# Performance work log

Hardware: AMD Instinct MI355X
Metric: run time of the kernel (lower is better)

The kernel has to match this reference:

```python
import jax, jax.numpy as jnp
import numpy as np

D = 128          # fine voxel grid resolution
N0 = 250000
D_IN, D_BASE, D_OUT = 16, 8, 8
EPS = 1e-5
# (cin, cout) for conv0..conv6, conv7, conv9, conv11
_CH = [(16, 8), (8, 16), (16, 16), (16, 32), (32, 32), (32, 64), (64, 64), (64, 32), (32, 16), (16, 8)]

def _offsets():
    r = np.arange(-1, 2)
    return np.stack(np.meshgrid(r, r, r, indexing='ij'), -1).reshape(-1, 3)  # [27,3]

def _lookup_fn(coords, d):
    keys = (coords[:, 0].astype(np.int64) * d + coords[:, 1]) * d + coords[:, 2]
    order = np.argsort(keys)
    skeys = keys[order]
    def lookup(q):
        valid = ((q >= 0) & (q < d)).all(-1)
        k = (q[:, 0].astype(np.int64) * d + q[:, 1]) * d + q[:, 2]
        pos = np.clip(np.searchsorted(skeys, k), 0, len(skeys) - 1)
        return np.where(valid & (skeys[pos] == k), order[pos], -1).astype(np.int32)
    return lookup

def _nbr_same(coords, d):
    # stride-1 sparse conv: outputs at input coords, neighbors at coord+k
    lk = _lookup_fn(coords, d)
    return np.stack([lk(coords + o) for o in _offsets()], 1)  # [N,27]

def _nbr_down(c_out, c_in, d_in):
    # stride-2 conv: output p gathers inputs at 2p+k
    lk = _lookup_fn(c_in, d_in)
    return np.stack([lk(c_out * 2 + o) for o in _offsets()], 1)

def _nbr_up(c_out, c_in, d_in):
    # transposed stride-2 conv: output q gathers input p=(q-k)/2 where divisible
    lk = _lookup_fn(c_in, d_in)
    cols = []
    for o in _offsets():
        q = c_out - o
        div = (q % 2 == 0).all(-1)
        cols.append(np.where(div, lk(q // 2), -1).astype(np.int32))
    return np.stack(cols, 1)

def setup_inputs():
    rng = np.random.default_rng(0)
    flat = rng.choice(D ** 3, size=N0, replace=False)
    c0 = np.stack([flat // (D * D), (flat // D) % D, flat % D], 1).astype(np.int32)
    c1 = np.unique(c0 // 2, axis=0)
    c2 = np.unique(c1 // 2, axis=0)
    c3 = np.unique(c2 // 2, axis=0)
    inp = {
        'feats': jax.random.normal(jax.random.key(0), (N0, D_IN), jnp.float32),
        'nbr0': jnp.asarray(_nbr_same(c0, D)),
        'nbr_d01': jnp.asarray(_nbr_down(c1, c0, D)),
        'nbr1': jnp.asarray(_nbr_same(c1, D // 2)),
        'nbr_d12': jnp.asarray(_nbr_down(c2, c1, D // 2)),
        'nbr2': jnp.asarray(_nbr_same(c2, D // 4)),
        'nbr_d23': jnp.asarray(_nbr_down(c3, c2, D // 4)),
        'nbr3': jnp.asarray(_nbr_same(c3, D // 8)),
        'nbr_u32': jnp.asarray(_nbr_up(c2, c3, D // 8)),
        'nbr_u21': jnp.asarray(_nbr_up(c1, c2, D // 4)),
        'nbr_u10': jnp.asarray(_nbr_up(c0, c1, D // 2)),
    }
    key = jax.random.key(1)
    for i, (ci, co) in enumerate(_CH):
        key, kw = jax.random.split(key)
        inp['w%d' % i] = jax.random.normal(kw, (27, ci, co), jnp.float32) / np.sqrt(27.0 * ci)
        inp['g%d' % i] = jnp.ones((co,), jnp.float32)
        inp['b%d' % i] = jnp.zeros((co,), jnp.float32)
    inp['lin_w'] = jax.random.normal(jax.random.key(2), (D_OUT, D_BASE), jnp.float32) / np.sqrt(D_BASE)
    return inp

def _sconv_bn_relu(f, nbr, w, g, b):
    # f: [Nin,Cin], nbr: [Nout,27] (-1 = no neighbor), w: [27,Cin,Cout]
    gth = jnp.where((nbr >= 0)[..., None], f[jnp.maximum(nbr, 0)], 0.0)  # [Nout,27,Cin]
    y = jnp.einsum('nkc,kco->no', gth, w)
    mu = y.mean(0)                       # training-mode BatchNorm over active voxels
    var = y.var(0)
    return jax.nn.relu((y - mu) * jax.lax.rsqrt(var + EPS) * g + b)

def reference(feats, nbr0, nbr_d01, nbr1, nbr_d12, nbr2, nbr_d23, nbr3, nbr_u32, nbr_u21, nbr_u10,
              w0, g0, b0, w1, g1, b1, w2, g2, b2, w3, g3, b3, w4, g4, b4,
              w5, g5, b5, w6, g6, b6, w7, g7, b7, w8, g8, b8, w9, g9, b9, lin_w):
    c0f = _sconv_bn_relu(feats, nbr0, w0, g0, b0)
    c2f = _sconv_bn_relu(_sconv_bn_relu(c0f, nbr_d01, w1, g1, b1), nbr1, w2, g2, b2)
    c4f = _sconv_bn_relu(_sconv_bn_relu(c2f, nbr_d12, w3, g3, b3), nbr2, w4, g4, b4)
    x = _sconv_bn_relu(_sconv_bn_relu(c4f, nbr_d23, w5, g5, b5), nbr3, w6, g6, b6)
    x = c4f + _sconv_bn_relu(x, nbr_u32, w7, g7, b7)
    x = c2f + _sconv_bn_relu(x, nbr_u21, w8, g8, b8)
    x = c0f + _sconv_bn_relu(x, nbr_u10, w9, g9, b9)
    return x @ lin_w.T, x
```

## Files before the change

### kernel.cpp

```cpp
#include <hip/hip_runtime.h>

#define EPSV 1e-5f

typedef __attribute__((ext_vector_type(8))) short short8;
typedef __attribute__((ext_vector_type(4))) float float4v;

static inline int cdiv(int a, int b) { return (a + b - 1) / b; }
static inline int imin(int a, int b) { return a < b ? a : b; }

__device__ inline unsigned short f2bf(float x) {
  unsigned u = __float_as_uint(x);
  return (unsigned short)((u + 0x7FFFu + ((u >> 16) & 1u)) >> 16);
}
__device__ inline float bf2f(unsigned short u) {
  return __uint_as_float(((unsigned)u) << 16);
}

#define NBUCKET 64

struct PrepArgs {
  const float* w[10];
  unsigned short* wt[10];
  int ci[10];
  int co[10];
  int wcum[11];
  const float* feats;
  unsigned short* featsb;
  int nfeat4;
  float* stats;
};

__global__ __launch_bounds__(256) void prep_kernel(PrepArgs p, long total) {
  const int nstat4 = 10 * NBUCKET * 128 / 4;
  for (long tid0 = (long)blockIdx.x * 256 + threadIdx.x; tid0 < total;
       tid0 += (long)gridDim.x * 256) {
    long tid = tid0;
    if (tid < nstat4) {
      ((float4*)p.stats)[tid] = make_float4(0.f, 0.f, 0.f, 0.f);
      continue;
    }
    tid -= nstat4;
    if (tid < p.nfeat4) {
      float4 v = ((const float4*)p.feats)[tid];
      ushort4 r;
      r.x = f2bf(v.x); r.y = f2bf(v.y); r.z = f2bf(v.z); r.w = f2bf(v.w);
      ((ushort4*)p.featsb)[tid] = r;
      continue;
    }
    tid -= p.nfeat4;
    if (tid >= p.wcum[10]) continue;
    int i = 0;
    while (tid >= p.wcum[i + 1]) ++i;
    int e = (int)(tid - p.wcum[i]);
    int ci = p.ci[i], co = p.co[i];
    int k = e / (ci * co);
    int r = e - k * (ci * co);
    int o = r / ci;
    int c = r - o * ci;
    p.wt[i][((long)k * co + o) * ci + c] = f2bf(p.w[i][((long)k * ci + c) * co + o]);
  }
}

template<int CI, int CO>
__global__ __launch_bounds__(256) void conv_mfma(
    const unsigned short* __restrict__ f, const int* __restrict__ nbr,
    const unsigned short* __restrict__ wt, unsigned short* __restrict__ y,
    float* __restrict__ stats, int nout, int ntiles) {
  constexpr int NCHUNK = (CI == 8) ? 7 : (CI == 16) ? 14 : (CI == 32) ? 27 : 54;

  const int tid = threadIdx.x;
  const int lane = tid & 63;
  const int wid = tid >> 6;
  const int m = lane & 15;
  const int quad = lane >> 4;
  const int cbase = blockIdx.y * 16;
  const int co = cbase + m;
  const bool cok = co < CO;

  auto tapof = [&](int c) -> int {
    if constexpr (CI == 8) return c * 4 + quad;
    else if constexpr (CI == 16) return c * 2 + (quad >> 1);
    else if constexpr (CI == 32) return c;
    else return c >> 1;
  };
  auto cioof = [&](int c) -> int {
    if constexpr (CI == 8) return 0;
    else if constexpr (CI == 16) return (quad & 1) * 8;
    else if constexpr (CI == 32) return quad * 8;
    else return ((c & 1) << 5) + quad * 8;
  };

  float sum = 0.f, sq = 0.f;

  if constexpr (CI <= 16) {
    short8 Bv[NCHUNK];
#pragma unroll
    for (int c = 0; c < NCHUNK; ++c) {
      int tap = tapof(c);
      short8 bq;
#pragma unroll
      for (int q = 0; q < 8; ++q) bq[q] = 0;
      if (cok && tap < 27) bq = *(const short8*)(wt + ((long)tap * CO + co) * CI + cioof(c));
      Bv[c] = bq;
    }
    for (int tile = blockIdx.x; tile < ntiles; tile += gridDim.x) {
      const int rowb = tile * 64 + wid * 16;
      const int row = rowb + m;
      const bool rok = row < nout;
      int idxs[NCHUNK];
#pragma unroll
      for (int c = 0; c < NCHUNK; ++c) {
        int tap = tapof(c);
        idxs[c] = (rok && tap < 27) ? nbr[(long)row * 27 + tap] : -1;
      }
      short8 A[NCHUNK];
#pragma unroll
      for (int c = 0; c < NCHUNK; ++c) {
        short8 a;
#pragma unroll
        for (int q = 0; q < 8; ++q) a[q] = 0;
        if (idxs[c] >= 0) a = *(const short8*)(f + (long)idxs[c] * CI + cioof(c));
        A[c] = a;
      }
      float4v acc = {0.f, 0.f, 0.f, 0.f};
#pragma unroll
      for (int c = 0; c < NCHUNK; ++c)
        acc = __builtin_amdgcn_mfma_f32_16x16x32_bf16(A[c], Bv[c], acc, 0, 0, 0);
#pragma unroll
      for (int r = 0; r < 4; ++r) {
        float v = acc[r];
        int orow = rowb + quad * 4 + r;
        if (cok && orow < nout) y[(long)orow * CO + co] = f2bf(v);
        sum += v;
        sq = fmaf(v, v, sq);
      }
    }
  } else {
    constexpr int G = 9;
    constexpr int NG = NCHUNK / G;
    for (int tile = blockIdx.x; tile < ntiles; tile += gridDim.x) {
      const int rowb = tile * 64 + wid * 16;
      const int row = rowb + m;
      const bool rok = row < nout;
      int idxs[27];
#pragma unroll
      for (int t = 0; t < 27; ++t)
        idxs[t] = rok ? nbr[(long)row * 27 + t] : -1;

      short8 A[2][G], B[2][G];
      auto load_group = [&](int g, int bi) {
#pragma unroll
        for (int j = 0; j < G; ++j) {
          const int c = g * G + j;
          const int tap = tapof(c);
          short8 a, bq;
#pragma unroll
          for (int q = 0; q < 8; ++q) { a[q] = 0; bq[q] = 0; }
          int idx = idxs[tap];
          if (idx >= 0) a = *(const short8*)(f + (long)idx * CI + cioof(c));
          if (cok) bq = *(const short8*)(wt + ((long)tap * CO + co) * CI + cioof(c));
          A[bi][j] = a; B[bi][j] = bq;
        }
      };
      float4v acc = {0.f, 0.f, 0.f, 0.f};
      load_group(0, 0);
#pragma unroll
      for (int g = 0; g < NG; ++g) {
        const int cur = g & 1;
        if (g + 1 < NG) load_group(g + 1, cur ^ 1);
#pragma unroll
        for (int j = 0; j < G; ++j)
          acc = __builtin_amdgcn_mfma_f32_16x16x32_bf16(A[cur][j], B[cur][j], acc, 0, 0, 0);
      }
#pragma unroll
      for (int r = 0; r < 4; ++r) {
        float v = acc[r];
        int orow = rowb + quad * 4 + r;
        if (cok && orow < nout) y[(long)orow * CO + co] = f2bf(v);
        sum += v;
        sq = fmaf(v, v, sq);
      }
    }
  }

  sum += __shfl_xor(sum, 16); sq += __shfl_xor(sq, 16);
  sum += __shfl_xor(sum, 32); sq += __shfl_xor(sq, 32);
  if (quad == 0 && cok) {
    float* st = stats + ((((unsigned)blockIdx.x * 4 + wid) & (NBUCKET - 1)) << 7);
    atomicAdd(&st[co], sum);
    atomicAdd(&st[64 + co], sq);
  }
}

template<int CO>
__global__ __launch_bounds__(256) void bn_relu_bf16(
    const unsigned short* __restrict__ y, const float* __restrict__ stats,
    const float* __restrict__ g, const float* __restrict__ b,
    const unsigned short* __restrict__ skip, unsigned short* __restrict__ out,
    int nout, float inv_n) {
  __shared__ float sA[CO], sC[CO];
  if ((int)threadIdx.x < CO) {
    int o = threadIdx.x;
    float su = 0.f, sq = 0.f;
#pragma unroll 8
    for (int bk = 0; bk < NBUCKET; ++bk) {
      su += stats[bk * 128 + o];
      sq += stats[bk * 128 + 64 + o];
    }
    float mu = su * inv_n;
    float var = sq * inv_n - mu * mu;
    float a = g[o] * rsqrtf(var + EPSV);
    sA[o] = a;
    sC[o] = fmaf(-mu, a, b[o]);
  }
  __syncthreads();
  long total4 = (long)nout * CO / 4;
  for (long i4 = (long)blockIdx.x * 256 + threadIdx.x; i4 < total4;
       i4 += (long)gridDim.x * 256) {
    int o = (int)((i4 * 4) % CO);
    ushort4 v = ((const ushort4*)y)[i4];
    float vv[4] = {bf2f(v.x), bf2f(v.y), bf2f(v.z), bf2f(v.w)};
    unsigned short rr[4];
#pragma unroll
    for (int j = 0; j < 4; ++j) {
      float x = fmaxf(fmaf(vv[j], sA[o + j], sC[o + j]), 0.f);
      if (skip) x += bf2f(skip[i4 * 4 + j]);
      rr[j] = f2bf(x);
    }
    ushort4 r;
    r.x = rr[0]; r.y = rr[1]; r.z = rr[2]; r.w = rr[3];
    ((ushort4*)out)[i4] = r;
  }
}

__global__ __launch_bounds__(256) void tail_kernel(
    const unsigned short* __restrict__ c0f, const float* __restrict__ st9,
    const float* __restrict__ g9, const float* __restrict__ b9, float inv_n,
    const float* __restrict__ lin_w, const unsigned short* __restrict__ y9,
    float* __restrict__ out0, float* __restrict__ x0, int n0) {
  __shared__ float swl[64];
  __shared__ float sbn[16];
  if (threadIdx.x < 64) swl[threadIdx.x] = lin_w[threadIdx.x];
  if (threadIdx.x < 8) {
    int o = threadIdx.x;
    float su = 0.f, sq = 0.f;
#pragma unroll 8
    for (int bk = 0; bk < NBUCKET; ++bk) {
      su += st9[bk * 128 + o];
      sq += st9[bk * 128 + 64 + o];
    }
    float mu = su * inv_n;
    float var = sq * inv_n - mu * mu;
    float a = g9[o] * rsqrtf(var + EPSV);
    sbn[o] = a;
    sbn[8 + o] = fmaf(-mu, a, b9[o]);
  }
  __syncthreads();
  for (int n = blockIdx.x * 256 + threadIdx.x; n < n0; n += gridDim.x * 256) {
    const ushort4* pr = (const ushort4*)(y9 + (long)n * 8);
    ushort4 r0 = pr[0], r1 = pr[1];
    unsigned short rw[8] = {r0.x, r0.y, r0.z, r0.w, r1.x, r1.y, r1.z, r1.w};
    const ushort4* pc = (const ushort4*)(c0f + (long)n * 8);
    ushort4 c0 = pc[0], c1 = pc[1];
    unsigned short cs[8] = {c0.x, c0.y, c0.z, c0.w, c1.x, c1.y, c1.z, c1.w};
    float xv[8];
#pragma unroll
    for (int c = 0; c < 8; ++c)
      xv[c] = bf2f(cs[c]) + fmaxf(fmaf(bf2f(rw[c]), sbn[c], sbn[8 + c]), 0.f);
    *(float4*)(x0 + (long)n * 8) = make_float4(xv[0], xv[1], xv[2], xv[3]);
    *(float4*)(x0 + (long)n * 8 + 4) = make_float4(xv[4], xv[5], xv[6], xv[7]);
    float ov[8];
#pragma unroll
    for (int j = 0; j < 8; ++j) {
      float s = 0.f;
#pragma unroll
      for (int c = 0; c < 8; ++c) s = fmaf(xv[c], swl[j * 8 + c], s);
      ov[j] = s;
    }
    *(float4*)(out0 + (long)n * 8) = make_float4(ov[0], ov[1], ov[2], ov[3]);
    *(float4*)(out0 + (long)n * 8 + 4) = make_float4(ov[4], ov[5], ov[6], ov[7]);
  }
}

extern "C" void kernel_launch(void* const* d_in, const int* in_sizes, int n_in,
                              void* d_out, int out_size, void* d_ws, size_t ws_size,
                              hipStream_t stream) {
  const float* feats   = (const float*)d_in[0];
  const int* nbr0      = (const int*)d_in[1];
  const int* nbr_d01   = (const int*)d_in[2];
  const int* nbr1      = (const int*)d_in[3];
  const int* nbr_d12   = (const int*)d_in[4];
  const int* nbr2      = (const int*)d_in[5];
  const int* nbr_d23   = (const int*)d_in[6];
  const int* nbr3      = (const int*)d_in[7];
  const int* nbr_u32   = (const int*)d_in[8];
  const int* nbr_u21   = (const int*)d_in[9];
  const int* nbr_u10   = (const int*)d_in[10];
  const float* w[10];
  const float* g[10];
  const float* b[10];
  for (int i = 0; i < 10; ++i) {
    w[i] = (const float*)d_in[11 + 3 * i];
    g[i] = (const float*)d_in[12 + 3 * i];
    b[i] = (const float*)d_in[13 + 3 * i];
  }
  const float* lin_w = (const float*)d_in[41];

  const int N0 = in_sizes[0] / 16;
  const int N1 = in_sizes[2] / 27;
  const int N2 = in_sizes[4] / 27;
  const int N3 = in_sizes[6] / 27;
  const float i0 = 1.f / N0, i1 = 1.f / N1, i2 = 1.f / N2, i3 = 1.f / N3;

  static const int CIv[10] = {16, 8, 16, 16, 32, 32, 64, 64, 32, 16};
  static const int COv[10] = {8, 16, 16, 32, 32, 64, 64, 32, 16, 8};

  float* stats = (float*)d_ws;
  unsigned short* u = (unsigned short*)(stats + 10 * NBUCKET * 128);

  unsigned short* yraw = u; u += (size_t)N1 * 32;

  unsigned short* wt[10];
  int wcum[11];
  wcum[0] = 0;
  for (int i = 0; i < 10; ++i) {
    wt[i] = u;
    int sz = 27 * CIv[i] * COv[i];
    u += sz;
    wcum[i + 1] = wcum[i] + sz;
  }
  unsigned short* featsb = u; u += (size_t)N0 * 16;
  unsigned short* c0f = u;    u += (size_t)N0 * 8;
  unsigned short* t1  = u;    u += (size_t)N1 * 16;
  unsigned short* c2f = u;    u += (size_t)N1 * 16;
  unsigned short* t2  = u;    u += (size_t)N2 * 32;
  unsigned short* c4f = u;    u += (size_t)N2 * 32;
  unsigned short* t3  = u;    u += (size_t)N3 * 64;
  unsigned short* t4  = u;    u += (size_t)N3 * 64;
  unsigned short* t5  = t2;
  unsigned short* t6  = t1;
  float* out0 = (float*)d_out;
  float* x0   = (float*)d_out + (size_t)N0 * 8;

  float* s[10];
  for (int i = 0; i < 10; ++i) s[i] = stats + i * NBUCKET * 128;

  PrepArgs pa;
  for (int i = 0; i < 10; ++i) {
    pa.w[i] = w[i]; pa.wt[i] = wt[i];
    pa.ci[i] = CIv[i]; pa.co[i] = COv[i];
    pa.wcum[i] = wcum[i];
  }
  pa.wcum[10] = wcum[10];
  pa.feats = feats; pa.featsb = featsb;
  pa.nfeat4 = N0 * 16 / 4;
  pa.stats = stats;
  long prep_total = (10 * NBUCKET * 128 / 4) + pa.nfeat4 + wcum[10];
  prep_kernel<<<imin((int)((prep_total + 255) / 256), 2048), 256, 0, stream>>>(pa, prep_total);

  auto bgrid = [](long nout, int co) {
    return imin((int)((nout * co / 4 + 255) / 256), 1024);
  };
  auto cgrid = [](int ntiles) { return imin(ntiles, 1024); };

  int tb0 = cdiv(N0, 64), tb1 = cdiv(N1, 64), tb2 = cdiv(N2, 64), tb3 = cdiv(N3, 64);

  conv_mfma<16, 8><<<dim3(cgrid(tb0), 1), 256, 0, stream>>>(featsb, nbr0, wt[0], yraw, s[0], N0, tb0);
  bn_relu_bf16<8><<<bgrid(N0, 8), 256, 0, stream>>>(yraw, s[0], g[0], b[0], nullptr, c0f, N0, i0);

  conv_mfma<8, 16><<<dim3(cgrid(tb1), 1), 256, 0, stream>>>(c0f, nbr_d01, wt[1], yraw, s[1], N1, tb1);
  bn_relu_bf16<16><<<bgrid(N1, 16), 256, 0, stream>>>(yraw, s[1], g[1], b[1], nullptr, t1, N1, i1);

  conv_mfma<16, 16><<<dim3(cgrid(tb1), 1), 256, 0, stream>>>(t1, nbr1, wt[2], yraw, s[2], N1, tb1);
  bn_relu_bf16<16><<<bgrid(N1, 16), 256, 0, stream>>>(yraw, s[2], g[2], b[2], nullptr, c2f, N1, i1);

  conv_mfma<16, 32><<<dim3(cgrid(tb2), 2), 256, 0, stream>>>(c2f, nbr_d12, wt[3], yraw, s[3], N2, tb2);
  bn_relu_bf16<32><<<bgrid(N2, 32), 256, 0, stream>>>(yraw, s[3], g[3], b[3], nullptr, t2, N2, i2);

  conv_mfma<32, 32><<<dim3(cgrid(tb2), 2), 256, 0, stream>>>(t2, nbr2, wt[4], yraw, s[4], N2, tb2);
  bn_relu_bf16<32><<<bgrid(N2, 32), 256, 0, stream>>>(yraw, s[4], g[4], b[4], nullptr, c4f, N2, i2);

  conv_mfma<32, 64><<<dim3(cgrid(tb3), 4), 256, 0, stream>>>(c4f, nbr_d23, wt[5], yraw, s[5], N3, tb3);
  bn_relu_bf16<64><<<bgrid(N3, 64), 256, 0, stream>>>(yraw, s[5], g[5], b[5], nullptr, t3, N3, i3);

  conv_mfma<64, 64><<<dim3(cgrid(tb3), 4), 256, 0, stream>>>(t3, nbr3, wt[6], yraw, s[6], N3, tb3);
  bn_relu_bf16<64><<<bgrid(N3, 64), 256, 0, stream>>>(yraw, s[6], g[6], b[6], nullptr, t4, N3, i3);

  conv_mfma<64, 32><<<dim3(cgrid(tb2), 2), 256, 0, stream>>>(t4, nbr_u32, wt[7], yraw, s[7], N2, tb2);
  bn_relu_bf16<32><<<bgrid(N2, 32), 256, 0, stream>>>(yraw, s[7], g[7], b[7], c4f, t5, N2, i2);

  conv_mfma<32, 16><<<dim3(cgrid(tb1), 1), 256, 0, stream>>>(t5, nbr_u21, wt[8], yraw, s[8], N1, tb1);
  bn_relu_bf16<16><<<bgrid(N1, 16), 256, 0, stream>>>(yraw, s[8], g[8], b[8], c2f, t6, N1, i1);

  conv_mfma<16, 8><<<dim3(cgrid(tb0), 1), 256, 0, stream>>>(t6, nbr_u10, wt[9], yraw, s[9], N0, tb0);

  tail_kernel<<<imin(cdiv(N0, 256), 1024), 256, 0, stream>>>(
      c0f, s[9], g[9], b[9], i0, lin_w, yraw, out0, x0, N0);
}
```

Measured before the change: 488.3 us.

## Stage conv weights and neighbor tiles in LDS, raise occupancy and grid size

The conv kernel now copies its slice of transposed weights into shared memory once per block, with an XOR swizzle for CI=64, and reads B fragments from LDS instead of keeping them in registers or reloading them from global memory on every tile. Each tile's 64x27 neighbor indices are loaded coalesced into shared memory with int4 loads. Launch bounds gain a per-instantiation min-waves hint and the conv grid cap rises from 1024 to 2048 blocks. In exchange it adds two __syncthreads per tile and LDS traffic, and the LDS footprint may limit occupancy.

```diff
diff --git a/kernel.cpp b/kernel.cpp
--- a/kernel.cpp
+++ b/kernel.cpp
@@ -61,12 +61,16 @@
   }
 }
 
-template<int CI, int CO>
-__global__ __launch_bounds__(256) void conv_mfma(
+template<int CI, int CO, int MINW>
+__global__ __launch_bounds__(256, MINW) void conv_mfma(
     const unsigned short* __restrict__ f, const int* __restrict__ nbr,
     const unsigned short* __restrict__ wt, unsigned short* __restrict__ y,
     float* __restrict__ stats, int nout, int ntiles) {
   constexpr int NCHUNK = (CI == 8) ? 7 : (CI == 16) ? 14 : (CI == 32) ? 27 : 54;
+  constexpr int CIP = (CI == 64) ? 64 : (CI == 32) ? 40 : 24;
+
+  __shared__ int nbrT[64 * 27];
+  __shared__ unsigned short Bs[27 * 16 * CIP];
 
   const int tid = threadIdx.x;
   const int lane = tid & 63;
@@ -89,29 +93,65 @@
     else if constexpr (CI == 32) return quad * 8;
     else return ((c & 1) << 5) + quad * 8;
   };
+  auto baddr = [&](int tap, int mm, int cio) -> int {
+    if constexpr (CI == 64) {
+      int byt = (tap * 16 + mm) * 128 + cio * 2;
+      byt ^= (mm & 7) << 4;
+      return byt >> 1;
+    } else {
+      return (tap * 16 + mm) * CIP + cio;
+    }
+  };
+
+  {
+    constexpr int NC8 = CI / 8;
+    for (int t = tid; t < 27 * 16 * NC8; t += 256) {
+      int tap = t / (16 * NC8);
+      int r = t - tap * (16 * NC8);
+      int mo = r / NC8;
+      int c8 = (r - mo * NC8) * 8;
+      short8 v;
+#pragma unroll
+      for (int q = 0; q < 8; ++q) v[q] = 0;
+      int c = cbase + mo;
+      if (c < CO) v = *(const short8*)(wt + ((long)tap * CO + c) * CI + c8);
+      *(short8*)&Bs[baddr(tap, mo, c8)] = v;
+    }
+  }
 
   float sum = 0.f, sq = 0.f;
 
-  if constexpr (CI <= 16) {
-    short8 Bv[NCHUNK];
-#pragma unroll
-    for (int c = 0; c < NCHUNK; ++c) {
-      int tap = tapof(c);
-      short8 bq;
-#pragma unroll
-      for (int q = 0; q < 8; ++q) bq[q] = 0;
-      if (cok && tap < 27) bq = *(const short8*)(wt + ((long)tap * CO + co) * CI + cioof(c));
-      Bv[c] = bq;
-    }
-    for (int tile = blockIdx.x; tile < ntiles; tile += gridDim.x) {
-      const int rowb = tile * 64 + wid * 16;
-      const int row = rowb + m;
-      const bool rok = row < nout;
+  for (int tile = blockIdx.x; tile < ntiles; tile += gridDim.x) {
+    const int rowb0 = tile * 64;
+    {
+      const int base = rowb0 * 27;
+      const int lim = nout * 27;
+      for (int j = tid; j < 432; j += 256) {
+        int e = j * 4;
+        int g = base + e;
+        int4 v;
+        if (g + 4 <= lim) {
+          v = *(const int4*)(nbr + g);
+        } else {
+          v.x = (g + 0 < lim) ? nbr[g + 0] : -1;
+          v.y = (g + 1 < lim) ? nbr[g + 1] : -1;
+          v.z = (g + 2 < lim) ? nbr[g + 2] : -1;
+          v.w = (g + 3 < lim) ? nbr[g + 3] : -1;
+        }
+        *(int4*)&nbrT[e] = v;
+      }
+    }
+    __syncthreads();
+
+    const int rowb = rowb0 + wid * 16;
+    const int lrow = (wid * 16 + m) * 27;
+
+    if constexpr (CI <= 16) {
       int idxs[NCHUNK];
 #pragma unroll
       for (int c = 0; c < NCHUNK; ++c) {
         int tap = tapof(c);
-        idxs[c] = (rok && tap < 27) ? nbr[(long)row * 27 + tap] : -1;
+        idxs[c] = (tap < 27) ? nbrT[lrow + tap] : -1;
       }
       short8 A[NCHUNK];
 #pragma unroll
@@ -124,8 +164,12 @@
       }
       float4v acc = {0.f, 0.f, 0.f, 0.f};
 #pragma unroll
-      for (int c = 0; c < NCHUNK; ++c)
-        acc = __builtin_amdgcn_mfma_f32_16x16x32_bf16(A[c], Bv[c], acc, 0, 0, 0);
+      for (int c = 0; c < NCHUNK; ++c) {
+        int tap = tapof(c);
+        int tapc = tap < 27 ? tap : 26;
+        short8 bf = *(const short8*)&Bs[baddr(tapc, m, cioof(c))];
+        acc = __builtin_amdgcn_mfma_f32_16x16x32_bf16(A[c], bf, acc, 0, 0, 0);
+      }
 #pragma unroll
       for (int r = 0; r < 4; ++r) {
         float v = acc[r];
@@ -134,32 +178,21 @@
         sum += v;
         sq = fmaf(v, v, sq);
       }
-    }
-  } else {
-    constexpr int G = 9;
-    constexpr int NG = NCHUNK / G;
-    for (int tile = blockIdx.x; tile < ntiles; tile += gridDim.x) {
-      const int rowb = tile * 64 + wid * 16;
-      const int row = rowb + m;
-      const bool rok = row < nout;
-      int idxs[27];
-#pragma unroll
-      for (int t = 0; t < 27; ++t)
-        idxs[t] = rok ? nbr[(long)row * 27 + t] : -1;
-
-      short8 A[2][G], B[2][G];
+    } else {
+      constexpr int G = 9;
+      constexpr int NG = NCHUNK / G;
+      short8 A[2][G];
       auto load_group = [&](int g, int bi) {
 #pragma unroll
         for (int j = 0; j < G; ++j) {
           const int c = g * G + j;
           const int tap = tapof(c);
-          short8 a, bq;
-#pragma unroll
-          for (int q = 0; q < 8; ++q) { a[q] = 0; bq[q] = 0; }
-          int idx = idxs[tap];
+          int idx = nbrT[lrow + tap];
+          short8 a;
+#pragma unroll
+          for (int q = 0; q < 8; ++q) a[q] = 0;
           if (idx >= 0) a = *(const short8*)(f + (long)idx * CI + cioof(c));
-          if (cok) bq = *(const short8*)(wt + ((long)tap * CO + co) * CI + cioof(c));
-          A[bi][j] = a; B[bi][j] = bq;
+          A[bi][j] = a;
         }
       };
       float4v acc = {0.f, 0.f, 0.f, 0.f};
@@ -169,8 +202,11 @@
         const int cur = g & 1;
         if (g + 1 < NG) load_group(g + 1, cur ^ 1);
 #pragma unroll
-        for (int j = 0; j < G; ++j)
-          acc = __builtin_amdgcn_mfma_f32_16x16x32_bf16(A[cur][j], B[cur][j], acc, 0, 0, 0);
+        for (int j = 0; j < G; ++j) {
+          const int c = g * G + j;
+          short8 bf = *(const short8*)&Bs[baddr(tapof(c), m, cioof(c))];
+          acc = __builtin_amdgcn_mfma_f32_16x16x32_bf16(A[cur][j], bf, acc, 0, 0, 0);
+        }
       }
 #pragma unroll
       for (int r = 0; r < 4; ++r) {
@@ -181,6 +217,7 @@
         sq = fmaf(v, v, sq);
       }
     }
+    __syncthreads();
   }
 
   sum += __shfl_xor(sum, 16); sq += __shfl_xor(sq, 16);
@@ -361,38 +398,38 @@
   auto bgrid = [](long nout, int co) {
     return imin((int)((nout * co / 4 + 255) / 256), 1024);
   };
-  auto cgrid = [](int ntiles) { return imin(ntiles, 1024); };
+  auto cgrid = [](int ntiles) { return imin(ntiles, 2048); };
 
   int tb0 = cdiv(N0, 64), tb1 = cdiv(N1, 64), tb2 = cdiv(N2, 64), tb3 = cdiv(N3, 64);
 
-  conv_mfma<16, 8><<<dim3(cgrid(tb0), 1), 256, 0, stream>>>(featsb, nbr0, wt[0], yraw, s[0], N0, tb0);
+  conv_mfma<16, 8, 4><<<dim3(cgrid(tb0), 1), 256, 0, stream>>>(featsb, nbr0, wt[0], yraw, s[0], N0, tb0);
   bn_relu_bf16<8><<<bgrid(N0, 8), 256, 0, stream>>>(yraw, s[0], g[0], b[0], nullptr, c0f, N0, i0);
 
-  conv_mfma<8, 16><<<dim3(cgrid(tb1), 1), 256, 0, stream>>>(c0f, nbr_d01, wt[1], yraw, s[1], N1, tb1);
+  conv_mfma<8, 16, 4><<<dim3(cgrid(tb1), 1), 256, 0, stream>>>(c0f, nbr_d01, wt[1], yraw, s[1], N1, tb1);
   bn_relu_bf16<16><<<bgrid(N1, 16), 256, 0, stream>>>(yraw, s[1], g[1], b[1], nullptr, t1, N1, i1);
 
-  conv_mfma<16, 16><<<dim3(cgrid(tb1), 1), 256, 0, stream>>>(t1, nbr1, wt[2], yraw, s[2], N1, tb1);
+  conv_mfma<16, 16, 4><<<dim3(cgrid(tb1), 1), 256, 0, stream>>>(t1, nbr1, wt[2], yraw, s[2], N1, tb1);
   bn_relu_bf16<16><<<bgrid(N1, 16), 256, 0, stream>>>(yraw, s[2], g[2], b[2], nullptr, c2f, N1, i1);
 
-  conv_mfma<16, 32><<<dim3(cgrid(tb2), 2), 256, 0, stream>>>(c2f, nbr_d12, wt[3], yraw, s[3], N2, tb2);
+  conv_mfma<16, 32, 4><<<dim3(cgrid(tb2), 2), 256, 0, stream>>>(c2f, nbr_d12, wt[3], yraw, s[3], N2, tb2);
   bn_relu_bf16<32><<<bgrid(N2, 32), 256, 0, stream>>>(yraw, s[3], g[3], b[3], nullptr, t2, N2, i2);
 
-  conv_mfma<32, 32><<<dim3(cgrid(tb2), 2), 256, 0, stream>>>(t2, nbr2, wt[4], yraw, s[4], N2, tb2);
+  conv_mfma<32, 32, 3><<<dim3(cgrid(tb2), 2), 256, 0, stream>>>(t2, nbr2, wt[4], yraw, s[4], N2, tb2);
   bn_relu_bf16<32><<<bgrid(N2, 32), 256, 0, stream>>>(yraw, s[4], g[4], b[4], nullptr, c4f, N2, i2);
 
-  conv_mfma<32, 64><<<dim3(cgrid(tb3), 4), 256, 0, stream>>>(c4f, nbr_d23, wt[5], yraw, s[5], N3, tb3);
+  conv_mfma<32, 64, 3><<<dim3(cgrid(tb3), 4), 256, 0, stream>>>(c4f, nbr_d23, wt[5], yraw, s[5], N3, tb3);
   bn_relu_bf16<64><<<bgrid(N3, 64), 256, 0, stream>>>(yraw, s[5], g[5], b[5], nullptr, t3, N3, i3);
 
-  conv_mfma<64, 64><<<dim3(cgrid(tb3), 4), 256, 0, stream>>>(t3, nbr3, wt[6], yraw, s[6], N3, tb3);
+  conv_mfma<64, 64, 2><<<dim3(cgrid(tb3), 4), 256, 0, stream>>>(t3, nbr3, wt[6], yraw, s[6], N3, tb3);
   bn_relu_bf16<64><<<bgrid(N3, 64), 256, 0, stream>>>(yraw, s[6], g[6], b[6], nullptr, t4, N3, i3);
 
-  conv_mfma<64, 32><<<dim3(cgrid(tb2), 2), 256, 0, stream>>>(t4, nbr_u32, wt[7], yraw, s[7], N2, tb2);
+  conv_mfma<64, 32, 2><<<dim3(cgrid(tb2), 2), 256, 0, stream>>>(t4, nbr_u32, wt[7], yraw, s[7], N2, tb2);
   bn_relu_bf16<32><<<bgrid(N2, 32), 256, 0, stream>>>(yraw, s[7], g[7], b[7], c4f, t5, N2, i2);
 
-  conv_mfma<32, 16><<<dim3(cgrid(tb1), 1), 256, 0, stream>>>(t5, nbr_u21, wt[8], yraw, s[8], N1, tb1);
+  conv_mfma<32, 16, 3><<<dim3(cgrid(tb1), 1), 256, 0, stream>>>(t5, nbr_u21, wt[8], yraw, s[8], N1, tb1);
   bn_relu_bf16<16><<<bgrid(N1, 16), 256, 0, stream>>>(yraw, s[8], g[8], b[8], c2f, t6, N1, i1);
 
-  conv_mfma<16, 8><<<dim3(cgrid(tb0), 1), 256, 0, stream>>>(t6, nbr_u10, wt[9], yraw, s[9], N0, tb0);
+  conv_mfma<16, 8, 4><<<dim3(cgrid(tb0), 1), 256, 0, stream>>>(t6, nbr_u10, wt[9], yraw, s[9], N0, tb0);
 
   tail_kernel<<<imin(cdiv(N0, 256), 1024), 256, 0, stream>>>(
       c0f, s[9], g[9], b[9], i0, lin_w, yraw, out0, x0, N0);
```

Measured after the change: 427.9 us. 12.4% less time.
